# Kernel tuning notes

Measured on AMD Instinct MI355X. Metric: run time of the kernel, lower is better.

The kernel has to match this reference:

```python
import jax, jax.numpy as jnp
import numpy as np

EPS = 1e-12


def setup_inputs() -> dict:
    key = jax.random.key(0)
    k1, k2, k3 = jax.random.split(key, 3)
    N, C = 2000000, 64
    x = jax.random.normal(k1, (N, C), dtype=jnp.float32)
    y = jax.random.randint(k2, (N,), 0, C, dtype=jnp.int64)
    obs = jax.random.uniform(k3, (N,), dtype=jnp.float32)
    return {"x": x, "y": y, "obs": obs}


def reference(x, y, obs):
    N, C = x.shape
    p = jnp.clip(jax.nn.softmax(x, axis=1), EPS)  # [N, C]
    # suffix[i, j] = sum_{k >= j} p[i, k]  (reverse cumsum)
    suffix = jnp.cumsum(p[:, ::-1], axis=1)[:, ::-1]
    p_y = jnp.take_along_axis(p, y[:, None], axis=1)[:, 0]  # p[i, y[i]]
    # sum over columns y[i]+1 .. C-1 (only used when y < C-1)
    idx_next = jnp.clip(y + 1, 0, C - 1)
    suf_y1 = jnp.take_along_axis(suffix, idx_next[:, None], axis=1)[:, 0]
    observed_term = jnp.log(p_y)
    censored_term = jnp.where(
        y == C - 1,
        jnp.log(jnp.clip(p_y, EPS)),
        jnp.log(jnp.clip(suf_y1, EPS)),
    )
    per_row = jnp.where(obs > 0.5, observed_term, censored_term)
    return -jnp.mean(per_row)
```

## Files before the change

kernel.cpp:

```cpp
#include <hip/hip_runtime.h>

#define EPS_F 1e-12f
constexpr int C = 64;
typedef float f32x4 __attribute__((ext_vector_type(4)));

__device__ __forceinline__ float process_row(f32x4 v, int yy, float ob, int sub) {
    float m = fmaxf(fmaxf(v.x, v.y), fmaxf(v.z, v.w));
    #pragma unroll
    for (int off = 1; off < 16; off <<= 1) m = fmaxf(m, __shfl_xor(m, off));

    const float e0 = __expf(v.x - m);
    const float e1 = __expf(v.y - m);
    const float e2 = __expf(v.z - m);
    const float e3 = __expf(v.w - m);
    float s = (e0 + e1) + (e2 + e3);
    #pragma unroll
    for (int off = 1; off < 16; off <<= 1) s += __shfl_xor(s, off);

    const float invZ = 1.0f / s;
    const float p0 = fmaxf(e0 * invZ, EPS_F);
    const float p1 = fmaxf(e1 * invZ, EPS_F);
    const float p2 = fmaxf(e2 * invZ, EPS_F);
    const float p3 = fmaxf(e3 * invZ, EPS_F);

    const int col0 = sub << 2;
    const bool use_py = (ob > 0.5f) || (yy == C - 1);

    float part = 0.f;
    if (use_py) {
        if (yy >= col0 && yy < col0 + 4) {
            const int r = yy - col0;
            part = (r == 0) ? p0 : (r == 1) ? p1 : (r == 2) ? p2 : p3;
        }
    } else {
        const int t = yy + 1;
        if (col0 + 0 >= t) part += p0;
        if (col0 + 1 >= t) part += p1;
        if (col0 + 2 >= t) part += p2;
        if (col0 + 3 >= t) part += p3;
    }
    #pragma unroll
    for (int off = 1; off < 16; off <<= 1) part += __shfl_xor(part, off);

    return __logf(fmaxf(part, EPS_F));
}

__global__ __launch_bounds__(256) void cce_main(const float* __restrict__ x,
                                                const int* __restrict__ y,
                                                const float* __restrict__ obs,
                                                double* __restrict__ ws_sum,
                                                int N) {
    const int tid  = threadIdx.x;
    const int lane = tid & 63;
    const int sub  = lane & 15;
    const int grp  = lane >> 4;
    const int waveInBlock   = tid >> 6;
    const int wavesPerBlock = blockDim.x >> 6;

    const long long NN         = N;
    const long long globalWave = (long long)blockIdx.x * wavesPerBlock + waveInBlock;
    const long long numWaves   = (long long)gridDim.x * wavesPerBlock;
    const long long numChunks  = (NN + 7) >> 3;

    float acc = 0.f;

    for (long long chunk = globalWave; chunk < numChunks; chunk += numWaves) {
        const long long row0 = chunk << 3;
        const long long rowA = row0 + grp;
        const long long rowB = row0 + 4 + grp;
        const bool vA = rowA < NN;
        const bool vB = rowB < NN;

        const f32x4* xv = reinterpret_cast<const f32x4*>(x + row0 * C);
        f32x4 a = {0.f, 0.f, 0.f, 0.f};
        f32x4 b = {0.f, 0.f, 0.f, 0.f};
        if (vA) a = __builtin_nontemporal_load(xv + lane);
        if (vB) b = __builtin_nontemporal_load(xv + 64 + lane);

        const int   yA = vA ? y[rowA]   : 0;
        const float oA = vA ? obs[rowA] : 1.f;
        const int   yB = vB ? y[rowB]   : 0;
        const float oB = vB ? obs[rowB] : 1.f;

        const float tA = process_row(a, yA, oA, sub);
        const float tB = process_row(b, yB, oB, sub);

        if (sub == 0) {
            if (vA) acc += tA;
            if (vB) acc += tB;
        }
    }

    #pragma unroll
    for (int off = 1; off < 64; off <<= 1) acc += __shfl_xor(acc, off);

    __shared__ float wsum[8];
    if (lane == 0) wsum[waveInBlock] = acc;
    __syncthreads();
    if (tid == 0) {
        float bsum = 0.f;
        for (int w = 0; w < wavesPerBlock; ++w) bsum += wsum[w];
        atomicAdd(ws_sum, (double)bsum);
    }
}

__global__ void cce_finalize(const double* __restrict__ ws_sum,
                             float* __restrict__ out, int N) {
    if (threadIdx.x == 0 && blockIdx.x == 0) {
        out[0] = (float)(-(*ws_sum) / (double)N);
    }
}

extern "C" void kernel_launch(void* const* d_in, const int* in_sizes, int n_in,
                              void* d_out, int out_size, void* d_ws, size_t ws_size,
                              hipStream_t stream) {
    const float* x   = (const float*)d_in[0];
    const int*   y   = (const int*)d_in[1];
    const float* obs = (const float*)d_in[2];
    int N = in_sizes[1];
    if (N <= 0) N = in_sizes[0] / C;

    double* ws_sum = (double*)d_ws;
    hipMemsetAsync(ws_sum, 0, sizeof(double), stream);

    const int block = 256;
    const long long chunks = ((long long)N + 7) >> 3;
    long long blocksNeeded = (chunks + 3) / 4;
    int grid = (int)((blocksNeeded < 2048) ? blocksNeeded : 2048);
    if (grid < 1) grid = 1;

    cce_main<<<grid, block, 0, stream>>>(x, y, obs, ws_sum, N);
    cce_finalize<<<1, 64, 0, stream>>>(ws_sum, (float*)d_out, N);
}
```

Baseline: 662.8 us.

## Use DPP for 16-lane reductions and process 16 rows per wave iteration

Replaces the __shfl_xor butterfly reductions (which go through ds_bpermute / LDS crossbar) with DPP row-level moves (quad_perm and row_shr) for the 16-lane max and sum reductions. Doubles the rows processed per wave iteration from 8 to 16, issuing four independent 16-byte loads up front on a fast path without bounds checks, plus a guarded tail path. The aim is to raise memory-level parallelism and cut the latency of the reductions. The cost is more registers per thread.

```diff
diff --git a/kernel.cpp b/kernel.cpp
--- a/kernel.cpp
+++ b/kernel.cpp
@@ -4,18 +4,34 @@
 constexpr int C = 64;
 typedef float f32x4 __attribute__((ext_vector_type(4)));
 
+template <int CTRL>
+__device__ __forceinline__ float dpp_movf(float v) {
+    return __int_as_float(__builtin_amdgcn_update_dpp(
+        0, __float_as_int(v), CTRL, 0xF, 0xF, false));
+}
+__device__ __forceinline__ float grp_max16(float v) {
+    v = fmaxf(v, dpp_movf<0xB1>(v));
+    v = fmaxf(v, dpp_movf<0x4E>(v));
+    v = fmaxf(v, dpp_movf<0x124>(v));
+    v = fmaxf(v, dpp_movf<0x128>(v));
+    return v;
+}
+__device__ __forceinline__ float grp_sum16(float v) {
+    v += dpp_movf<0xB1>(v);
+    v += dpp_movf<0x4E>(v);
+    v += dpp_movf<0x124>(v);
+    v += dpp_movf<0x128>(v);
+    return v;
+}
+
 __device__ __forceinline__ float process_row(f32x4 v, int yy, float ob, int sub) {
-    float m = fmaxf(fmaxf(v.x, v.y), fmaxf(v.z, v.w));
-    #pragma unroll
-    for (int off = 1; off < 16; off <<= 1) m = fmaxf(m, __shfl_xor(m, off));
+    float m = grp_max16(fmaxf(fmaxf(v.x, v.y), fmaxf(v.z, v.w)));
 
     const float e0 = __expf(v.x - m);
     const float e1 = __expf(v.y - m);
     const float e2 = __expf(v.z - m);
     const float e3 = __expf(v.w - m);
-    float s = (e0 + e1) + (e2 + e3);
-    #pragma unroll
-    for (int off = 1; off < 16; off <<= 1) s += __shfl_xor(s, off);
+    const float s  = grp_sum16((e0 + e1) + (e2 + e3));
 
     const float invZ = 1.0f / s;
     const float p0 = fmaxf(e0 * invZ, EPS_F);
@@ -39,9 +55,7 @@
         if (col0 + 2 >= t) part += p2;
         if (col0 + 3 >= t) part += p3;
     }
-    #pragma unroll
-    for (int off = 1; off < 16; off <<= 1) part += __shfl_xor(part, off);
-
+    part = grp_sum16(part);
     return __logf(fmaxf(part, EPS_F));
 }
 
@@ -60,34 +74,38 @@
     const long long NN         = N;
     const long long globalWave = (long long)blockIdx.x * wavesPerBlock + waveInBlock;
     const long long numWaves   = (long long)gridDim.x * wavesPerBlock;
-    const long long numChunks  = (NN + 7) >> 3;
+    const long long numChunks  = (NN + 15) >> 4;
 
     float acc = 0.f;
 
     for (long long chunk = globalWave; chunk < numChunks; chunk += numWaves) {
-        const long long row0 = chunk << 3;
-        const long long rowA = row0 + grp;
-        const long long rowB = row0 + 4 + grp;
-        const bool vA = rowA < NN;
-        const bool vB = rowB < NN;
+        const long long row0 = chunk << 4;
+        const f32x4* xv = reinterpret_cast<const f32x4*>(x + row0 * C);
 
-        const f32x4* xv = reinterpret_cast<const f32x4*>(x + row0 * C);
-        f32x4 a = {0.f, 0.f, 0.f, 0.f};
-        f32x4 b = {0.f, 0.f, 0.f, 0.f};
-        if (vA) a = __builtin_nontemporal_load(xv + lane);
-        if (vB) b = __builtin_nontemporal_load(xv + 64 + lane);
+        if (row0 + 16 <= NN) {
+            f32x4 a = __builtin_nontemporal_load(xv + lane);
+            f32x4 b = __builtin_nontemporal_load(xv + 64 + lane);
+            f32x4 c = __builtin_nontemporal_load(xv + 128 + lane);
+            f32x4 d = __builtin_nontemporal_load(xv + 192 + lane);
 
-        const int   yA = vA ? y[rowA]   : 0;
-        const float oA = vA ? obs[rowA] : 1.f;
-        const int   yB = vB ? y[rowB]   : 0;
-        const float oB = vB ? obs[rowB] : 1.f;
+            const int   yA = y[row0 + grp],        yB = y[row0 + 4 + grp];
+            const int   yC = y[row0 + 8 + grp],    yD = y[row0 + 12 + grp];
+            const float oA = obs[row0 + grp],      oB = obs[row0 + 4 + grp];
+            const float oC = obs[row0 + 8 + grp],  oD = obs[row0 + 12 + grp];
 
-        const float tA = process_row(a, yA, oA, sub);
-        const float tB = process_row(b, yB, oB, sub);
-
-        if (sub == 0) {
-            if (vA) acc += tA;
-            if (vB) acc += tB;
+            const float t = process_row(a, yA, oA, sub) + process_row(b, yB, oB, sub)
+                          + process_row(c, yC, oC, sub) + process_row(d, yD, oD, sub);
+            if (sub == 0) acc += t;
+        } else {
+            #pragma unroll
+            for (int p = 0; p < 4; ++p) {
+                const long long rowP = row0 + 4 * p + grp;
+                if (rowP < NN) {
+                    f32x4 v = __builtin_nontemporal_load(xv + 64 * p + lane);
+                    const float t = process_row(v, y[rowP], obs[rowP], sub);
+                    if (sub == 0) acc += t;
+                }
+            }
         }
     }
 
@@ -124,7 +142,7 @@
     hipMemsetAsync(ws_sum, 0, sizeof(double), stream);
 
     const int block = 256;
-    const long long chunks = ((long long)N + 7) >> 3;
+    const long long chunks = ((long long)N + 15) >> 4;
     long long blocksNeeded = (chunks + 3) / 4;
     int grid = (int)((blocksNeeded < 2048) ? blocksNeeded : 2048);
     if (grid < 1) grid = 1;
```

Result: faster. 648.5 us (-2.2%).
